# Performance work log

Hardware: AMD Instinct MI355X
Metric: run time of the kernel (lower is better)

Reference implementation:

```python
import jax, jax.numpy as jnp
import numpy as np

N_NODES = 100000
N_EDGES = 1600000
DIM = 128
HEADS = 8
PHC = DIM // HEADS  # per-head channels = 16


def setup_inputs() -> dict:
    key = jax.random.key(0)
    k1, k2, k3, k4, k5 = jax.random.split(key, 5)
    nodes = jax.random.normal(k1, (N_NODES, DIM), dtype=jnp.float32)
    senders = jax.random.randint(k2, (N_EDGES,), 0, N_NODES, dtype=jnp.int32)
    receivers = jax.random.randint(k3, (N_EDGES,), 0, N_NODES, dtype=jnp.int32)
    # VarianceScaling(fan_avg, uniform) ~ limit = sqrt(3/fan_avg)
    lim_w = np.sqrt(3.0 / DIM)
    W = jax.random.uniform(k4, (DIM, DIM), minval=-lim_w, maxval=lim_w, dtype=jnp.float32)
    b = jnp.zeros((DIM,), dtype=jnp.float32)
    lim_a = np.sqrt(3.0 * 2.0 / (2 * PHC + 1))
    attn_w = jax.random.uniform(k5, (2 * PHC, 1), minval=-lim_a, maxval=lim_a, dtype=jnp.float32)
    attn_b = jnp.zeros((1,), dtype=jnp.float32)
    return {"nodes": nodes, "senders": senders, "receivers": receivers,
            "W": W, "b": b, "attn_w": attn_w, "attn_b": attn_b}


def reference(nodes, senders, receivers, W, b, attn_w, attn_b):
    n = nodes.shape[0]
    # linear transform + split heads: [N, H, PHC]
    nt = (nodes @ W + b).reshape(n, HEADS, PHC)
    sent = nt[senders]      # [E, H, PHC] gather
    recv = nt[receivers]    # [E, H, PHC] gather
    # attention logits: Linear(1) over leaky_relu(concat(q,k)) -> [E, H, 1]
    qk = jax.nn.leaky_relu(jnp.concatenate([sent, recv], axis=-1), negative_slope=0.2)
    logits = qk @ attn_w + attn_b  # [E, H, 1]
    # segment softmax over edges grouped by receiver node
    seg_max = jax.ops.segment_max(logits, receivers, num_segments=n)  # [N, H, 1]
    exp = jnp.exp(logits - seg_max[receivers])
    denom = jax.ops.segment_sum(exp, receivers, num_segments=n)  # [N, H, 1]
    alpha = exp / denom[receivers]
    # weighted scatter-sum of sender features
    out = jax.ops.segment_sum(sent * alpha, receivers, num_segments=n)  # [N, H, PHC]
    return out.reshape(n, -1)  # concat=True -> [N, DIM]
```

## Files before the change

kernel.cpp:

```cpp
#include <hip/hip_runtime.h>

#define DIM 128
#define HEADS 8
#define PHC 16

#define BSHIFT 6
#define BNODES 64
#define CAP 1408
#define NBMAX 1600

typedef __bf16 bf16x4 __attribute__((ext_vector_type(4)));
typedef __bf16 bf16x8 __attribute__((ext_vector_type(8)));
typedef float  f32x4  __attribute__((ext_vector_type(4)));

__device__ inline unsigned short f2bf(float x) {
  unsigned int u = __float_as_uint(x);
  unsigned int r = (u + 0x7FFF + ((u >> 16) & 1)) >> 16;
  return (unsigned short)r;
}

__global__ __launch_bounds__(256) void k_prepw(
    const float* __restrict__ W, __bf16* __restrict__ Wh,
    __bf16* __restrict__ Wl) {
  const int tuple = blockIdx.x * 256 + threadIdx.x;
  const int ln = tuple & 15;
  const int lg = (tuple >> 4) & 3;
  const int cg = (tuple >> 6) & 7;
  const int kt = tuple >> 9;
  const int col = (cg << 4) + ln;
  bf16x8 h, l;
#pragma unroll
  for (int e = 0; e < 8; ++e) {
    int k = (kt << 5) + ((e >> 2) << 4) + (lg << 2) + (e & 3);
    float wv = W[k * DIM + col];
    __bf16 hh = (__bf16)wv;
    h[e] = hh;
    l[e] = (__bf16)(wv - (float)hh);
  }
  *(bf16x8*)(Wh + tuple * 8) = h;
  *(bf16x8*)(Wl + tuple * 8) = l;
}

#define GROWS 64

__global__ __launch_bounds__(256, 3) void k_gemm(
    const float* __restrict__ A, const __bf16* __restrict__ Wh,
    const __bf16* __restrict__ Wl, const float* __restrict__ bias,
    const float* __restrict__ attn_w, unsigned int* __restrict__ nt_bf,
    float* __restrict__ s_exp, int* __restrict__ gCursor, int NB, int n) {
  __shared__ __align__(16) float smemF[GROWS * DIM];
  __bf16* Ah = (__bf16*)smemF;
  __bf16* Al = Ah + GROWS * DIM;
  const int t    = threadIdx.x;
  const int row0 = blockIdx.x * GROWS;
  const int lane = t & 63;
  const int w    = t >> 6;
  const int lg   = lane >> 4;
  const int ln   = lane & 15;

  if (blockIdx.x == 0)
    for (int i = t; i < NB; i += 256) gCursor[i] = 0;

  float4 av[8];
  {
    const float4* A4 = (const float4*)(A + (size_t)row0 * DIM);
    const int lim = min(GROWS, n - row0) * (DIM / 4);
#pragma unroll
    for (int j = 0; j < 8; ++j) {
      int i = t + j * 256;
      av[j] = (i < lim) ? A4[i] : make_float4(0.f, 0.f, 0.f, 0.f);
    }
  }

#pragma unroll
  for (int j = 0; j < 8; ++j) {
    int i = t + j * 256;
    int r = i >> 5, c4 = i & 31;
    int ktc = c4 >> 3, lgc = c4 & 3, ehi = (c4 >> 2) & 1;
    int unit = (r << 4) + (((ktc << 2) + lgc) ^ (r & 15));
    int ei = (unit << 3) + (ehi << 2);
    float x0 = av[j].x, x1 = av[j].y, x2 = av[j].z, x3 = av[j].w;
    __bf16 h0 = (__bf16)x0, h1 = (__bf16)x1, h2 = (__bf16)x2, h3 = (__bf16)x3;
    bf16x4 hv = {h0, h1, h2, h3};
    bf16x4 lv = {(__bf16)(x0 - (float)h0), (__bf16)(x1 - (float)h1),
                 (__bf16)(x2 - (float)h2), (__bf16)(x3 - (float)h3)};
    *(bf16x4*)(Ah + ei) = hv;
    *(bf16x4*)(Al + ei) = lv;
  }

  f32x4 acc[4][2];
  {
    const float b0 = bias[(w << 5) + ln];
    const float b1 = bias[(w << 5) + 16 + ln];
#pragma unroll
    for (int rt = 0; rt < 4; ++rt) {
      acc[rt][0] = (f32x4){b0, b0, b0, b0};
      acc[rt][1] = (f32x4){b1, b1, b1, b1};
    }
  }
  __syncthreads();

  const int cg0 = w << 1;
#pragma unroll
  for (int kt = 0; kt < 4; ++kt) {
    bf16x8 Bh0, Bl0, Bh1, Bl1;
    {
      int i0 = ((((kt << 3) + cg0) << 2) + lg) * 16 + ln;
      int i1 = ((((kt << 3) + cg0 + 1) << 2) + lg) * 16 + ln;
      Bh0 = *(const bf16x8*)(Wh + (i0 << 3));
      Bl0 = *(const bf16x8*)(Wl + (i0 << 3));
      Bh1 = *(const bf16x8*)(Wh + (i1 << 3));
      Bl1 = *(const bf16x8*)(Wl + (i1 << 3));
    }
    bf16x8 ah[4], al[4];
#pragma unroll
    for (int rt = 0; rt < 4; ++rt) {
      int m = (rt << 4) + ln;
      int u = (m << 4) + (((kt << 2) + lg) ^ (m & 15));
      ah[rt] = *(const bf16x8*)(Ah + (u << 3));
      al[rt] = *(const bf16x8*)(Al + (u << 3));
    }
#pragma unroll
    for (int rt = 0; rt < 4; ++rt) {
      acc[rt][0] = __builtin_amdgcn_mfma_f32_16x16x32_bf16(ah[rt], Bh0, acc[rt][0], 0, 0, 0);
      acc[rt][0] = __builtin_amdgcn_mfma_f32_16x16x32_bf16(ah[rt], Bl0, acc[rt][0], 0, 0, 0);
      acc[rt][0] = __builtin_amdgcn_mfma_f32_16x16x32_bf16(al[rt], Bh0, acc[rt][0], 0, 0, 0);
      acc[rt][1] = __builtin_amdgcn_mfma_f32_16x16x32_bf16(ah[rt], Bh1, acc[rt][1], 0, 0, 0);
      acc[rt][1] = __builtin_amdgcn_mfma_f32_16x16x32_bf16(ah[rt], Bl1, acc[rt][1], 0, 0, 0);
      acc[rt][1] = __builtin_amdgcn_mfma_f32_16x16x32_bf16(al[rt], Bh1, acc[rt][1], 0, 0, 0);
    }
  }

  __syncthreads();

#pragma unroll
  for (int rt = 0; rt < 4; ++rt)
#pragma unroll
    for (int ct = 0; ct < 2; ++ct) {
      int colx = ((w << 5) + (ct << 4) + ln) ^ ((lg & 1) << 4);
#pragma unroll
      for (int r = 0; r < 4; ++r) {
        int rowl = (rt << 4) + (lg << 2) + r;
        smemF[(rowl << 7) + colx] = acc[rt][ct][r];
      }
    }

  {
    const float aw = attn_w[ln];
#pragma unroll
    for (int rt = 0; rt < 4; ++rt)
#pragma unroll
      for (int ct = 0; ct < 2; ++ct) {
        const int head = (w << 1) + ct;
#pragma unroll
        for (int r = 0; r < 4; ++r) {
          float v = acc[rt][ct][r];
          float p = (v > 0.f ? v : 0.2f * v) * aw;
          p += __shfl_xor(p, 1);
          p += __shfl_xor(p, 2);
          p += __shfl_xor(p, 4);
          p += __shfl_xor(p, 8);
          if (ln == 0) {
            int row = row0 + (rt << 4) + (lg << 2) + r;
            if (row < n) s_exp[row * HEADS + head] = __expf(p);
          }
        }
      }
  }
  __syncthreads();

  {
    const int nrow = min(GROWS, n - row0);
#pragma unroll
    for (int j = 0; j < 8; ++j) {
      int i = t + j * 256;
      int r = i >> 5, c4 = i & 31;
      if (r < nrow) {
        int c4s = c4 ^ (((r >> 2) & 1) << 2);
        f32x4 v = *(const f32x4*)(smemF + (r << 7) + (c4s << 2));
        unsigned int lo = (unsigned int)f2bf(v[0]) | ((unsigned int)f2bf(v[1]) << 16);
        unsigned int hi = (unsigned int)f2bf(v[2]) | ((unsigned int)f2bf(v[3]) << 16);
        ((uint2*)nt_bf)[(size_t)(row0 + r) * 32 + c4] = make_uint2(lo, hi);
      }
    }
  }
}

__global__ __launch_bounds__(256) void k_scatterpairs(
    const int* __restrict__ send, const int* __restrict__ recv,
    int* __restrict__ gCursor, unsigned int* __restrict__ pairs,
    int E, int NB) {
  __shared__ int cnt[NBMAX];
  __shared__ int cur[NBMAX];
  const int t = threadIdx.x;
  for (int i = t; i < NB; i += 256) cnt[i] = 0;
  __syncthreads();
  const int e0 = blockIdx.x * 8192;
  const int e1 = min(e0 + 8192, E);
  for (int i = e0 + t; i < e1; i += 256)
    atomicAdd(&cnt[recv[i] >> BSHIFT], 1);
  __syncthreads();
  for (int i = t; i < NB; i += 256) {
    int c = cnt[i];
    cur[i] = i * CAP + (c ? atomicAdd(&gCursor[i], c) : 0);
  }
  __syncthreads();
  for (int i = e0 + t; i < e1; i += 256) {
    int r = recv[i];
    int b = r >> BSHIFT;
    int p = atomicAdd(&cur[b], 1);
    if (p - b * CAP < CAP)
      pairs[p] = (unsigned int)send[i] | ((unsigned int)(r & (BNODES - 1)) << 17);
  }
}

__device__ inline void acc8(float wgt, uint4 qv, float4& a0, float4& a1) {
  a0.x = fmaf(wgt, __uint_as_float(qv.x << 16), a0.x);
  a0.y = fmaf(wgt, __uint_as_float(qv.x & 0xFFFF0000u), a0.y);
  a0.z = fmaf(wgt, __uint_as_float(qv.y << 16), a0.z);
  a0.w = fmaf(wgt, __uint_as_float(qv.y & 0xFFFF0000u), a0.w);
  a1.x = fmaf(wgt, __uint_as_float(qv.z << 16), a1.x);
  a1.y = fmaf(wgt, __uint_as_float(qv.z & 0xFFFF0000u), a1.y);
  a1.z = fmaf(wgt, __uint_as_float(qv.w << 16), a1.z);
  a1.w = fmaf(wgt, __uint_as_float(qv.w & 0xFFFF0000u), a1.w);
}

__global__ __launch_bounds__(256) void k_aggbuild(
    const unsigned int* __restrict__ pairs, const int* __restrict__ gCursor,
    const unsigned int* __restrict__ nt_bf, const float* __restrict__ s_exp,
    float* __restrict__ out, int n) {
  __shared__ unsigned int buf[CAP];
  __shared__ int csr_l[CAP];
  __shared__ int hist[BNODES], offl[BNODES], curl[BNODES];
  const int b = blockIdx.x;
  const int t = threadIdx.x;
  const int base = b * CAP;
  const int bsize = min(gCursor[b], CAP);

  for (int i = t; i < bsize; i += 256) buf[i] = pairs[base + i];
  if (t < BNODES) hist[t] = 0;
  __syncthreads();
  for (int i = t; i < bsize; i += 256)
    atomicAdd(&hist[(buf[i] >> 17) & (BNODES - 1)], 1);
  __syncthreads();
  if (t < 64) {
    int v = hist[t];
    int x = v;
#pragma unroll
    for (int off = 1; off < 64; off <<= 1) {
      int y = __shfl_up(x, off);
      if (t >= off) x += y;
    }
    offl[t] = x - v;
    curl[t] = x - v;
  }
  __syncthreads();
  for (int i = t; i < bsize; i += 256) {
    unsigned int v = buf[i];
    int p = atomicAdd(&curl[(v >> 17) & (BNODES - 1)], 1);
    csr_l[p] = (int)(v & 0x1FFFF);
  }
  __syncthreads();

  const int wv   = t >> 6;
  const int lane = t & 63;
  const int q    = lane >> 4;
  const int l16  = lane & 15;
  const int head = l16 >> 1;
  const uint4* nt4 = (const uint4*)nt_bf;

#pragma unroll 1
  for (int pi = 0; pi < 4; ++pi) {
    const int nl = wv * 16 + pi * 4 + q;
    const int node = (b << BSHIFT) + nl;
    const int deg = hist[nl];
    const int eoff = offl[nl];
    float4 a0 = make_float4(0.f, 0.f, 0.f, 0.f);
    float4 a1 = make_float4(0.f, 0.f, 0.f, 0.f);
    float den = 0.f;
    for (int j = 0; j < deg; j += 4) {
      bool ok1 = (j + 1) < deg, ok2 = (j + 2) < deg, ok3 = (j + 3) < deg;
      int s0 = csr_l[eoff + j];
      int s1 = csr_l[ok1 ? (eoff + j + 1) : eoff];
      int s2 = csr_l[ok2 ? (eoff + j + 2) : eoff];
      int s3 = csr_l[ok3 ? (eoff + j + 3) : eoff];
      float w0 = s_exp[s0 * HEADS + head];
      float w1 = ok1 ? s_exp[s1 * HEADS + head] : 0.f;
      float w2 = ok2 ? s_exp[s2 * HEADS + head] : 0.f;
      float w3 = ok3 ? s_exp[s3 * HEADS + head] : 0.f;
      uint4 q0 = nt4[(size_t)s0 * 16 + l16];
      uint4 q1 = nt4[(size_t)s1 * 16 + l16];
      uint4 q2 = nt4[(size_t)s2 * 16 + l16];
      uint4 q3 = nt4[(size_t)s3 * 16 + l16];
      den += (w0 + w1) + (w2 + w3);
      acc8(w0, q0, a0, a1);
      acc8(w1, q1, a0, a1);
      acc8(w2, q2, a0, a1);
      acc8(w3, q3, a0, a1);
    }
    if (node < n) {
      const float inv = (deg > 0) ? 1.0f / den : 0.f;
      float4* op = (float4*)out + (size_t)node * 32 + l16 * 2;
      op[0] = make_float4(a0.x * inv, a0.y * inv, a0.z * inv, a0.w * inv);
      op[1] = make_float4(a1.x * inv, a1.y * inv, a1.z * inv, a1.w * inv);
    }
  }
}

extern "C" void kernel_launch(void* const* d_in, const int* in_sizes, int n_in,
                              void* d_out, int out_size, void* d_ws, size_t ws_size,
                              hipStream_t stream) {
  const float* nodes   = (const float*)d_in[0];
  const int*   senders = (const int*)d_in[1];
  const int*   recvs   = (const int*)d_in[2];
  const float* W       = (const float*)d_in[3];
  const float* bias    = (const float*)d_in[4];
  const float* attn_w  = (const float*)d_in[5];

  const int n = in_sizes[0] / DIM;
  const int E = in_sizes[1];
  const int NB = (n + BNODES - 1) >> BSHIFT;

  char* w = (char*)d_ws;
  auto align256 = [](size_t x) { return (x + 255) & ~(size_t)255; };
  size_t off = 0;
  unsigned int* nt_bf = (unsigned int*)(w + off); off += align256((size_t)n * DIM * 2);
  float* s_exp   = (float*)(w + off); off += align256((size_t)n * HEADS * 4);
  unsigned int* pairs = (unsigned int*)(w + off); off += align256((size_t)NB * CAP * 4);
  int* gCursor   = (int*)(w + off);   off += align256((size_t)NB * 4);
  __bf16* Wh     = (__bf16*)(w + off); off += align256((size_t)2048 * 8 * 2);
  __bf16* Wl     = (__bf16*)(w + off); off += align256((size_t)2048 * 8 * 2);
  (void)ws_size;

  k_prepw<<<8, 256, 0, stream>>>(W, Wh, Wl);
  k_gemm<<<(n + GROWS - 1) / GROWS, 256, 0, stream>>>(nodes, Wh, Wl, bias, attn_w,
                                                      nt_bf, s_exp, gCursor, NB, n);
  const int nb1 = (E + 8191) / 8192;
  k_scatterpairs<<<nb1, 256, 0, stream>>>(senders, recvs, gCursor, pairs, E, NB);
  k_aggbuild<<<NB, 256, 0, stream>>>(pairs, gCursor, nt_bf, s_exp,
                                     (float*)d_out, n);
}
```

Baseline: 268.2 us.

## Fuse edge bucketing into GEMM launch and split aggregation across head halves

Moves the gCursor reset into the weight-prep kernel and merges the edge-scatter pass into the GEMM launch as extra leading blocks, so bucketing runs concurrently with the GEMM and one launch is removed. The aggregation kernel now launches two blocks per 64-node bucket, each handling half the heads, which doubles parallelism but makes each block rebuild the local CSR redundantly. The scatter blocks reuse the GEMM's shared memory, so block occupancy follows the larger GEMM footprint.

```diff
diff --git a/kernel.cpp b/kernel.cpp
--- a/kernel.cpp
+++ b/kernel.cpp
@@ -21,8 +21,9 @@
 
 __global__ __launch_bounds__(256) void k_prepw(
     const float* __restrict__ W, __bf16* __restrict__ Wh,
-    __bf16* __restrict__ Wl) {
+    __bf16* __restrict__ Wl, int* __restrict__ gCursor, int NB) {
   const int tuple = blockIdx.x * 256 + threadIdx.x;
+  if (tuple < NB) gCursor[tuple] = 0;
   const int ln = tuple & 15;
   const int lg = (tuple >> 4) & 3;
   const int cg = (tuple >> 6) & 7;
@@ -43,23 +44,49 @@
 
 #define GROWS 64
 
-__global__ __launch_bounds__(256, 3) void k_gemm(
+__global__ __launch_bounds__(256, 3) void k_gemm_scatter(
     const float* __restrict__ A, const __bf16* __restrict__ Wh,
     const __bf16* __restrict__ Wl, const float* __restrict__ bias,
     const float* __restrict__ attn_w, unsigned int* __restrict__ nt_bf,
-    float* __restrict__ s_exp, int* __restrict__ gCursor, int NB, int n) {
+    float* __restrict__ s_exp, const int* __restrict__ send,
+    const int* __restrict__ recv, int* __restrict__ gCursor,
+    unsigned int* __restrict__ pairs, int E, int NB, int nScat, int n) {
   __shared__ __align__(16) float smemF[GROWS * DIM];
+
+  if (blockIdx.x < nScat) {
+    int* cnt = (int*)smemF;
+    int* cur = cnt + NBMAX;
+    const int t = threadIdx.x;
+    for (int i = t; i < NB; i += 256) cnt[i] = 0;
+    __syncthreads();
+    const int e0 = blockIdx.x * 8192;
+    const int e1 = min(e0 + 8192, E);
+    for (int i = e0 + t; i < e1; i += 256)
+      atomicAdd(&cnt[recv[i] >> BSHIFT], 1);
+    __syncthreads();
+    for (int i = t; i < NB; i += 256) {
+      int c = cnt[i];
+      cur[i] = i * CAP + (c ? atomicAdd(&gCursor[i], c) : 0);
+    }
+    __syncthreads();
+    for (int i = e0 + t; i < e1; i += 256) {
+      int r = recv[i];
+      int b = r >> BSHIFT;
+      int p = atomicAdd(&cur[b], 1);
+      if (p - b * CAP < CAP)
+        pairs[p] = (unsigned int)send[i] | ((unsigned int)(r & (BNODES - 1)) << 17);
+    }
+    return;
+  }
+
   __bf16* Ah = (__bf16*)smemF;
   __bf16* Al = Ah + GROWS * DIM;
   const int t    = threadIdx.x;
-  const int row0 = blockIdx.x * GROWS;
+  const int row0 = (blockIdx.x - nScat) * GROWS;
   const int lane = t & 63;
   const int w    = t >> 6;
   const int lg   = lane >> 4;
   const int ln   = lane & 15;
-
-  if (blockIdx.x == 0)
-    for (int i = t; i < NB; i += 256) gCursor[i] = 0;
 
   float4 av[8];
   {
@@ -186,34 +213,6 @@
   }
 }
 
-__global__ __launch_bounds__(256) void k_scatterpairs(
-    const int* __restrict__ send, const int* __restrict__ recv,
-    int* __restrict__ gCursor, unsigned int* __restrict__ pairs,
-    int E, int NB) {
-  __shared__ int cnt[NBMAX];
-  __shared__ int cur[NBMAX];
-  const int t = threadIdx.x;
-  for (int i = t; i < NB; i += 256) cnt[i] = 0;
-  __syncthreads();
-  const int e0 = blockIdx.x * 8192;
-  const int e1 = min(e0 + 8192, E);
-  for (int i = e0 + t; i < e1; i += 256)
-    atomicAdd(&cnt[recv[i] >> BSHIFT], 1);
-  __syncthreads();
-  for (int i = t; i < NB; i += 256) {
-    int c = cnt[i];
-    cur[i] = i * CAP + (c ? atomicAdd(&gCursor[i], c) : 0);
-  }
-  __syncthreads();
-  for (int i = e0 + t; i < e1; i += 256) {
-    int r = recv[i];
-    int b = r >> BSHIFT;
-    int p = atomicAdd(&cur[b], 1);
-    if (p - b * CAP < CAP)
-      pairs[p] = (unsigned int)send[i] | ((unsigned int)(r & (BNODES - 1)) << 17);
-  }
-}
-
 __device__ inline void acc8(float wgt, uint4 qv, float4& a0, float4& a1) {
   a0.x = fmaf(wgt, __uint_as_float(qv.x << 16), a0.x);
   a0.y = fmaf(wgt, __uint_as_float(qv.x & 0xFFFF0000u), a0.y);
@@ -232,7 +231,8 @@
   __shared__ unsigned int buf[CAP];
   __shared__ int csr_l[CAP];
   __shared__ int hist[BNODES], offl[BNODES], curl[BNODES];
-  const int b = blockIdx.x;
+  const int b = blockIdx.x >> 1;
+  const int c = blockIdx.x & 1;
   const int t = threadIdx.x;
   const int base = b * CAP;
   const int bsize = min(gCursor[b], CAP);
@@ -264,14 +264,15 @@
 
   const int wv   = t >> 6;
   const int lane = t & 63;
-  const int q    = lane >> 4;
-  const int l16  = lane & 15;
-  const int head = l16 >> 1;
+  const int e8   = lane >> 3;
+  const int l8   = lane & 7;
+  const int head = (c << 2) + (l8 >> 1);
+  const int uoff = (c << 3) + l8;
   const uint4* nt4 = (const uint4*)nt_bf;
 
 #pragma unroll 1
-  for (int pi = 0; pi < 4; ++pi) {
-    const int nl = wv * 16 + pi * 4 + q;
+  for (int pi = 0; pi < 2; ++pi) {
+    const int nl = (wv << 4) + (pi << 3) + e8;
     const int node = (b << BSHIFT) + nl;
     const int deg = hist[nl];
     const int eoff = offl[nl];
@@ -288,10 +289,10 @@
       float w1 = ok1 ? s_exp[s1 * HEADS + head] : 0.f;
       float w2 = ok2 ? s_exp[s2 * HEADS + head] : 0.f;
       float w3 = ok3 ? s_exp[s3 * HEADS + head] : 0.f;
-      uint4 q0 = nt4[(size_t)s0 * 16 + l16];
-      uint4 q1 = nt4[(size_t)s1 * 16 + l16];
-      uint4 q2 = nt4[(size_t)s2 * 16 + l16];
-      uint4 q3 = nt4[(size_t)s3 * 16 + l16];
+      uint4 q0 = nt4[(size_t)s0 * 16 + uoff];
+      uint4 q1 = nt4[(size_t)s1 * 16 + uoff];
+      uint4 q2 = nt4[(size_t)s2 * 16 + uoff];
+      uint4 q3 = nt4[(size_t)s3 * 16 + uoff];
       den += (w0 + w1) + (w2 + w3);
       acc8(w0, q0, a0, a1);
       acc8(w1, q1, a0, a1);
@@ -300,7 +301,7 @@
     }
     if (node < n) {
       const float inv = (deg > 0) ? 1.0f / den : 0.f;
-      float4* op = (float4*)out + (size_t)node * 32 + l16 * 2;
+      float4* op = (float4*)out + (size_t)node * 32 + (c << 4) + (l8 << 1);
       op[0] = make_float4(a0.x * inv, a0.y * inv, a0.z * inv, a0.w * inv);
       op[1] = make_float4(a1.x * inv, a1.y * inv, a1.z * inv, a1.w * inv);
     }
@@ -332,11 +333,12 @@
   __bf16* Wl     = (__bf16*)(w + off); off += align256((size_t)2048 * 8 * 2);
   (void)ws_size;
 
-  k_prepw<<<8, 256, 0, stream>>>(W, Wh, Wl);
-  k_gemm<<<(n + GROWS - 1) / GROWS, 256, 0, stream>>>(nodes, Wh, Wl, bias, attn_w,
-                                                      nt_bf, s_exp, gCursor, NB, n);
-  const int nb1 = (E + 8191) / 8192;
-  k_scatterpairs<<<nb1, 256, 0, stream>>>(senders, recvs, gCursor, pairs, E, NB);
-  k_aggbuild<<<NB, 256, 0, stream>>>(pairs, gCursor, nt_bf, s_exp,
-                                     (float*)d_out, n);
-}
+  k_prepw<<<8, 256, 0, stream>>>(W, Wh, Wl, gCursor, NB);
+  const int nScat = (E + 8191) / 8192;
+  const int ngemm = (n + GROWS - 1) / GROWS;
+  k_gemm_scatter<<<nScat + ngemm, 256, 0, stream>>>(
+      nodes, Wh, Wl, bias, attn_w, nt_bf, s_exp,
+      senders, recvs, gCursor, pairs, E, NB, nScat, n);
+  k_aggbuild<<<NB * 2, 256, 0, stream>>>(pairs, gCursor, nt_bf, s_exp,
+                                         (float*)d_out, n);
+}
```

Result: faster. 252.1 us (-6.0%).
